# Optimization experiments

Measured on AMD Instinct MI355X. Metric: run time of the kernel, lower is better.

The kernel has to match this reference:

```python
import jax, jax.numpy as jnp
import numpy as np

B, S, D, H = 2, 2048, 1024, 16
DK = D // H

def setup_inputs() -> dict:
    key = jax.random.key(0)
    ks = jax.random.split(key, 11)
    s = 1.0 / np.sqrt(D)
    inp = {
        'q': jax.random.normal(ks[0], (B, S, D), jnp.float32),
        'k': jax.random.normal(ks[1], (B, S, D), jnp.float32),
        'v': jax.random.normal(ks[2], (B, S, D), jnp.float32),
        'mask': jnp.tril(jnp.ones((S, S), jnp.bool_))[None, None],  # [1,1,S,S] causal
        'w_q': jax.random.normal(ks[3], (D, D), jnp.float32) * s,
        'b_q': jax.random.normal(ks[4], (D,), jnp.float32) * s,
        'w_k': jax.random.normal(ks[5], (D, D), jnp.float32) * s,
        'b_k': jax.random.normal(ks[6], (D,), jnp.float32) * s,
        'w_v': jax.random.normal(ks[7], (D, D), jnp.float32) * s,
        'b_v': jax.random.normal(ks[8], (D,), jnp.float32) * s,
        'w_o': jax.random.normal(ks[9], (D, D), jnp.float32) * s,
        'b_o': jax.random.normal(ks[10], (D,), jnp.float32) * s,
    }
    return inp

def reference(q, k, v, mask, w_q, b_q, w_k, b_k, w_v, b_v, w_o, b_o):
    # Linear projections (torch Linear: x @ W^T + b)
    qh = (q @ w_q.T + b_q).reshape(B, S, H, DK).transpose(0, 2, 1, 3)  # [B,H,S,DK]
    kh = (k @ w_k.T + b_k).reshape(B, S, H, DK).transpose(0, 2, 1, 3)
    vh = (v @ w_v.T + b_v).reshape(B, S, H, DK).transpose(0, 2, 1, 3)
    scores = jnp.einsum('bhqd,bhkd->bhqk', qh, kh) / jnp.sqrt(jnp.float32(DK))
    scores = jnp.where(mask, scores, jnp.float32(-jnp.inf))
    attn = jax.nn.softmax(scores, axis=-1)  # dropout p=0.0 -> identity
    out = jnp.einsum('bhqk,bhkd->bhqd', attn, vh)
    out = out.transpose(0, 2, 1, 3).reshape(B, S, D)
    return out @ w_o.T + b_o
```

## Files before the change

kernel.cpp:

```cpp
#include <hip/hip_runtime.h>
#include <hip/hip_bf16.h>

typedef __bf16 bf16_t;
typedef __bf16 bf16x4 __attribute__((ext_vector_type(4)));
typedef __bf16 bf16x8 __attribute__((ext_vector_type(8)));
typedef float f32x4 __attribute__((ext_vector_type(4)));

#define B_ 2
#define S_ 2048
#define D_ 1024
#define H_ 16
#define DK_ 64
#define M_ (B_ * S_)

__device__ __forceinline__ f32x4 mfma16(bf16x8 a, bf16x8 b, f32x4 c) {
  return __builtin_amdgcn_mfma_f32_16x16x32_bf16(a, b, c, 0, 0, 0);
}

__device__ __forceinline__ void async_load16(const bf16_t* g, bf16_t* l) {
  __builtin_amdgcn_global_load_lds(
      (const __attribute__((address_space(1))) void*)g,
      (__attribute__((address_space(3))) void*)l, 16, 0, 0);
}


__global__ void cvt_all(const float* __restrict__ q, const float* __restrict__ k,
                        const float* __restrict__ v, const float* __restrict__ w0,
                        const float* __restrict__ w1, const float* __restrict__ w2,
                        const float* __restrict__ w3, bf16_t* __restrict__ qb,
                        bf16_t* __restrict__ kb, bf16_t* __restrict__ vb,
                        bf16_t* __restrict__ o0, bf16_t* __restrict__ o1,
                        bf16_t* __restrict__ o2, bf16_t* __restrict__ o3) {
  const int y = blockIdx.y;
  if (y >= 3 && blockIdx.x >= 512) return;
  const float* src;
  bf16_t* dst;
  float sc = 1.0f;
  switch (y) {
    case 0: src = q; dst = qb; break;
    case 1: src = k; dst = kb; break;
    case 2: src = v; dst = vb; break;
    case 3: src = w0; dst = o0; sc = 0.125f; break;
    case 4: src = w1; dst = o1; break;
    case 5: src = w2; dst = o2; break;
    default: src = w3; dst = o3; break;
  }
  long i = ((long)blockIdx.x * blockDim.x + threadIdx.x) * 8;
  const float4* s4 = (const float4*)(src + i);
  float4 a = s4[0], b = s4[1];
  bf16x8 o;
  o[0] = (bf16_t)(a.x * sc); o[1] = (bf16_t)(a.y * sc);
  o[2] = (bf16_t)(a.z * sc); o[3] = (bf16_t)(a.w * sc);
  o[4] = (bf16_t)(b.x * sc); o[5] = (bf16_t)(b.y * sc);
  o[6] = (bf16_t)(b.z * sc); o[7] = (bf16_t)(b.w * sc);
  *(bf16x8*)(dst + i) = o;
}


__device__ __forceinline__ int swzG(int b) {
  return b ^ (((b >> 7) & 7) << 4);
}

template <int NR>
__device__ __forceinline__ void stage_tile(const bf16_t* g, bf16_t* lds,
                                           const int* srcoff, int wave) {
#pragma unroll
  for (int rnd = 0; rnd < NR; ++rnd)
    async_load16(g + srcoff[rnd], lds + rnd * 2048 + wave * 512);
}

template <int MODE>
__device__ __forceinline__ void gemm_core(const bf16_t* __restrict__ A,
                                          const bf16_t* __restrict__ W,
                                          const float* __restrict__ bias,
                                          float bscale, void* __restrict__ Cv,
                                          bf16_t* __restrict__ As,
                                          bf16_t* __restrict__ Bs) {
  constexpr int N = 1024, K = 1024;
  constexpr int TILE = 128 * 64;
  const int tid = threadIdx.x;
  const int wave = tid >> 6, lane = tid & 63;
  const int quad = lane >> 4, l15 = lane & 15;
  const int wm = wave >> 1, wn = wave & 1;
  const int bm = blockIdx.x * 128, bn = blockIdx.y * 128;

  f32x4 acc[4][4] = {};

  int srcoff[4];
#pragma unroll
  for (int rnd = 0; rnd < 4; ++rnd) {
    const int bb = rnd * 4096 + tid * 16;
    const int sb = swzG(bb);
    srcoff[rnd] = (sb >> 7) * K + ((sb & 127) >> 1);
  }
  const bf16_t* ag = A + (long)bm * K;
  const bf16_t* bg = W + (long)bn * K;

  const int co0 = ((quad * 16) ^ ((l15 & 7) << 4)) >> 1;
  const int co1 = ((quad * 16 + 64) ^ ((l15 & 7) << 4)) >> 1;
  const int arow0 = (wm * 64 + l15) * 64;
  const int brow0 = (wn * 64 + l15) * 64;

  stage_tile<4>(ag, As, srcoff, wave);
  stage_tile<4>(bg, Bs, srcoff, wave);

  int cur = 0;
  for (int kk = 0; kk < K; kk += 64) {
    if (kk + 64 < K) {
      stage_tile<4>(ag + kk + 64, As + (cur ^ 1) * TILE, srcoff, wave);
      stage_tile<4>(bg + kk + 64, Bs + (cur ^ 1) * TILE, srcoff, wave);
      asm volatile("s_waitcnt vmcnt(8)" ::: "memory");
    } else {
      asm volatile("s_waitcnt vmcnt(0)" ::: "memory");
    }
    __builtin_amdgcn_sched_barrier(0);
    __builtin_amdgcn_s_barrier();
    __builtin_amdgcn_sched_barrier(0);

    const bf16_t* Ac = As + cur * TILE;
    const bf16_t* Bc = Bs + cur * TILE;
#pragma unroll
    for (int h = 0; h < 2; ++h) {
      const int co = h ? co1 : co0;
      bf16x8 af[4], bfr[4];
#pragma unroll
      for (int i = 0; i < 4; ++i)
        af[i] = *(const bf16x8*)&Ac[arow0 + i * 1024 + co];
#pragma unroll
      for (int i = 0; i < 4; ++i)
        bfr[i] = *(const bf16x8*)&Bc[brow0 + i * 1024 + co];
      __builtin_amdgcn_s_setprio(1);
#pragma unroll
      for (int mi = 0; mi < 4; ++mi)
#pragma unroll
        for (int ni = 0; ni < 4; ++ni)
          acc[mi][ni] = mfma16(af[mi], bfr[ni], acc[mi][ni]);
      __builtin_amdgcn_s_setprio(0);
    }

    asm volatile("s_waitcnt lgkmcnt(0)" ::: "memory");
    __builtin_amdgcn_sched_barrier(0);
    __builtin_amdgcn_s_barrier();
    __builtin_amdgcn_sched_barrier(0);
    cur ^= 1;
  }

#pragma unroll
  for (int mi = 0; mi < 4; ++mi) {
#pragma unroll
    for (int ni = 0; ni < 4; ++ni) {
      const int col = bn + wn * 64 + ni * 16 + l15;
      const float bsv = bias[col] * bscale;
      f32x4 v = acc[mi][ni];
      const int row0 = bm + wm * 64 + mi * 16 + quad * 4;
      if (MODE == 3) {
        float* C = (float*)Cv;
#pragma unroll
        for (int r = 0; r < 4; ++r)
          C[(long)(row0 + r) * N + col] = v[r] + bsv;
      } else if (MODE == 1) {
        bf16_t* C = (bf16_t*)Cv;
        const int hh = col >> 6, dk = col & 63;
        const int bq = row0 >> 11, s0 = row0 & 2047;
        bf16_t* base = C + (((long)bq * H_ + hh) * S_ + s0) * DK_ + dk;
#pragma unroll
        for (int r = 0; r < 4; ++r)
          base[(long)r * DK_] = (bf16_t)(v[r] + bsv);
      } else {
        bf16_t* C = (bf16_t*)Cv;
        const int hh = col >> 6, dk = col & 63;
        const int bq = row0 >> 11, s0 = row0 & 2047;
        bf16x4 pk;
#pragma unroll
        for (int r = 0; r < 4; ++r) pk[r] = (bf16_t)(v[r] + bsv);
        *(bf16x4*)(C + (((long)bq * H_ + hh) * DK_ + dk) * S_ + s0) = pk;
      }
    }
  }
}

__global__ __launch_bounds__(256) void gemm_qkv(
    const bf16_t* __restrict__ qb, const bf16_t* __restrict__ kb,
    const bf16_t* __restrict__ vb, const bf16_t* __restrict__ wq,
    const bf16_t* __restrict__ wk, const bf16_t* __restrict__ wv,
    const float* __restrict__ biq, const float* __restrict__ bik,
    const float* __restrict__ biv, bf16_t* __restrict__ Qh,
    bf16_t* __restrict__ Kh, bf16_t* __restrict__ Vt) {
  __shared__ bf16_t As[2][128 * 64];
  __shared__ bf16_t Bs[2][128 * 64];
  if (blockIdx.z == 0)
    gemm_core<1>(qb, wq, biq, 0.125f, Qh, &As[0][0], &Bs[0][0]);
  else if (blockIdx.z == 1)
    gemm_core<1>(kb, wk, bik, 1.0f, Kh, &As[0][0], &Bs[0][0]);
  else
    gemm_core<2>(vb, wv, biv, 1.0f, Vt, &As[0][0], &Bs[0][0]);
}

__global__ __launch_bounds__(256) void gemm_out64(
    const bf16_t* __restrict__ AO, const bf16_t* __restrict__ wo,
    const float* __restrict__ bo, float* __restrict__ out) {
  constexpr int N = 1024, K = 1024;
  __shared__ bf16_t As[2][64 * 64];
  __shared__ bf16_t Bs[2][128 * 64];
  const int tid = threadIdx.x;
  const int wave = tid >> 6, lane = tid & 63;
  const int quad = lane >> 4, l15 = lane & 15;
  const int wm = wave >> 1, wn = wave & 1;
  const int bm = blockIdx.x * 64, bn = blockIdx.y * 128;

  f32x4 acc[2][4] = {};

  int srcoff[4];
#pragma unroll
  for (int rnd = 0; rnd < 4; ++rnd) {
    const int bb = rnd * 4096 + tid * 16;
    const int sb = swzG(bb);
    srcoff[rnd] = (sb >> 7) * K + ((sb & 127) >> 1);
  }
  const bf16_t* ag = AO + (long)bm * K;
  const bf16_t* bg = wo + (long)bn * K;

  const int co0 = ((quad * 16) ^ ((l15 & 7) << 4)) >> 1;
  const int co1 = ((quad * 16 + 64) ^ ((l15 & 7) << 4)) >> 1;
  const int arow0 = (wm * 32 + l15) * 64;
  const int brow0 = (wn * 64 + l15) * 64;

  stage_tile<2>(ag, &As[0][0], srcoff, wave);
  stage_tile<4>(bg, &Bs[0][0], srcoff, wave);

  int cur = 0;
  for (int kk = 0; kk < K; kk += 64) {
    if (kk + 64 < K) {
      stage_tile<2>(ag + kk + 64, &As[cur ^ 1][0], srcoff, wave);
      stage_tile<4>(bg + kk + 64, &Bs[cur ^ 1][0], srcoff, wave);
      asm volatile("s_waitcnt vmcnt(6)" ::: "memory");
    } else {
      asm volatile("s_waitcnt vmcnt(0)" ::: "memory");
    }
    __builtin_amdgcn_sched_barrier(0);
    __builtin_amdgcn_s_barrier();
    __builtin_amdgcn_sched_barrier(0);

#pragma unroll
    for (int h = 0; h < 2; ++h) {
      const int co = h ? co1 : co0;
      bf16x8 af[2], bfr[4];
#pragma unroll
      for (int i = 0; i < 2; ++i)
        af[i] = *(const bf16x8*)&As[cur][arow0 + i * 1024 + co];
#pragma unroll
      for (int i = 0; i < 4; ++i)
        bfr[i] = *(const bf16x8*)&Bs[cur][brow0 + i * 1024 + co];
      __builtin_amdgcn_s_setprio(1);
#pragma unroll
      for (int mi = 0; mi < 2; ++mi)
#pragma unroll
        for (int ni = 0; ni < 4; ++ni)
          acc[mi][ni] = mfma16(af[mi], bfr[ni], acc[mi][ni]);
      __builtin_amdgcn_s_setprio(0);
    }

    asm volatile("s_waitcnt lgkmcnt(0)" ::: "memory");
    __builtin_amdgcn_sched_barrier(0);
    __builtin_amdgcn_s_barrier();
    __builtin_amdgcn_sched_barrier(0);
    cur ^= 1;
  }

#pragma unroll
  for (int mi = 0; mi < 2; ++mi) {
#pragma unroll
    for (int ni = 0; ni < 4; ++ni) {
      const int col = bn + wn * 64 + ni * 16 + l15;
      const float bsv = bo[col];
      f32x4 v = acc[mi][ni];
      const int row0 = bm + wm * 32 + mi * 16 + quad * 4;
#pragma unroll
      for (int r = 0; r < 4; ++r)
        out[(long)(row0 + r) * N + col] = v[r] + bsv;
    }
  }
}


__device__ __forceinline__ int swzK(int b) {
  return b ^ (((b >> 7) & 3) << 4) ^ (((b >> 10) & 1) << 6);
}
__device__ __forceinline__ int swzV(int b) {
  return b ^ (((b >> 7) & 7) << 4);
}

template <bool MASKED>
__device__ __forceinline__ void softmax_pa(const f32x4 st[4], float& l_i,
                                           bf16x8& pa0, bf16x8& pa1,
                                           const int qcol, const int quad) {
#pragma unroll
  for (int nb = 0; nb < 4; ++nb) {
    const int kvb = quad * 8 + (nb & 1) * 4 + (nb >> 1) * 32;
#pragma unroll
    for (int r = 0; r < 4; ++r) {
      float x = st[nb][r];
      if (MASKED && (kvb + r) > qcol) x = -30000.f;
      const float pv = __expf(x);
      l_i += pv;
      const bf16_t pb = (bf16_t)pv;
      const int idx = ((nb & 1) << 2) | r;
      if (nb < 2) pa0[idx] = pb;
      else        pa1[idx] = pb;
    }
  }
}

__global__ __launch_bounds__(256, 3) void flash_attn3(
    const bf16_t* __restrict__ Qh, const bf16_t* __restrict__ Kh,
    const bf16_t* __restrict__ Vt, bf16_t* __restrict__ Po,
    float* __restrict__ Pl) {
  const int bid = blockIdx.x;
  const int g = bid & 31;
  const int z = bid >> 5;
  const int i = z / 3, pi = z % 3;
  const int h = g & 15, b = g >> 4;
  const int tA = i, tB = 31 - i;
  const int tid = threadIdx.x, wave = tid >> 6, lane = tid & 63;
  const int quad = lane >> 4, l15 = lane & 15;
  const int qcol = wave * 16 + l15;
  const int prow = ((l15 >> 2) << 3) | (l15 & 3);

  __shared__ bf16_t Kls[2][64 * 64];
  __shared__ bf16_t Vls[2][64 * 64];

  const bf16_t* qhead = Qh + ((long)(b * H_ + h) * S_) * DK_;
  const bf16_t* khead = Kh + ((long)(b * H_ + h) * S_) * DK_;
  const bf16_t* vhead = Vt + ((long)(b * H_ + h) * DK_) * S_;

  int koffe[2], voffe[2], ldse[2];
#pragma unroll
  for (int c = 0; c < 2; ++c) {
    const int bb = c * 4096 + wave * 1024 + lane * 16;
    koffe[c] = swzK(bb) >> 1;
    const int vs = swzV(bb);
    voffe[c] = (vs >> 7) * S_ + ((vs & 127) >> 1);
    ldse[c] = c * 2048 + wave * 512;
  }

  int kro[4][2], vro[4][2];
#pragma unroll
  for (int nb = 0; nb < 4; ++nb) {
    const int krow = prow + (nb & 1) * 4 + (nb >> 1) * 32;
    const int vrow = nb * 16 + l15;
#pragma unroll
    for (int hh = 0; hh < 2; ++hh) {
      kro[nb][hh] = swzK(krow * 128 + quad * 16 + hh * 64) >> 1;
      vro[nb][hh] = swzV(vrow * 128 + quad * 16 + hh * 64) >> 1;
    }
  }

  const int qA = tA * 64 + wave * 16;
  const int qB = tB * 64 + wave * 16;
  const bf16_t* qpA = qhead + (long)(qA + l15) * DK_ + quad * 8;
  const bf16_t* qpB = qhead + (long)(qB + l15) * DK_ + quad * 8;
  const bf16x8 aqA0 = *(const bf16x8*)qpA;
  const bf16x8 aqA1 = *(const bf16x8*)(qpA + 32);
  const bf16x8 aqB0 = *(const bf16x8*)qpB;
  const bf16x8 aqB1 = *(const bf16x8*)(qpB + 32);

  f32x4 oA[4] = {}, oB[4] = {};
  float lA = 0.f, lB = 0.f;

  {
    const bf16_t* kt = khead + pi * (64 * DK_);
    const bf16_t* vt = vhead + pi * 64;
#pragma unroll
    for (int c = 0; c < 2; ++c) {
      async_load16(kt + koffe[c], &Kls[0][ldse[c]]);
      async_load16(vt + voffe[c], &Vls[0][ldse[c]]);
    }
  }

  int cur = 0;
  for (int j = pi; j <= tB; j += 3) {
    const bool pf = (j + 3 <= tB);
    if (pf) {
      const bf16_t* kt = khead + (j + 3) * (64 * DK_);
      const bf16_t* vt = vhead + (j + 3) * 64;
#pragma unroll
      for (int c = 0; c < 2; ++c) {
        async_load16(kt + koffe[c], &Kls[cur ^ 1][ldse[c]]);
        async_load16(vt + voffe[c], &Vls[cur ^ 1][ldse[c]]);
      }
      asm volatile("s_waitcnt vmcnt(4)" ::: "memory");
    } else {
      asm volatile("s_waitcnt vmcnt(0)" ::: "memory");
    }
    __builtin_amdgcn_sched_barrier(0);
    __builtin_amdgcn_s_barrier();
    __builtin_amdgcn_sched_barrier(0);

    const bf16_t* Kc = &Kls[cur][0];
    const bf16_t* Vc = &Vls[cur][0];

    bf16x8 k0[4], k1[4];
#pragma unroll
    for (int nb = 0; nb < 4; ++nb) {
      k0[nb] = *(const bf16x8*)&Kc[kro[nb][0]];
      k1[nb] = *(const bf16x8*)&Kc[kro[nb][1]];
    }

    bf16x8 paB0, paB1, paA0, paA1;
    {
      f32x4 stB[4];
#pragma unroll
      for (int nb = 0; nb < 4; ++nb) {
        f32x4 t = {};
        t = mfma16(k0[nb], aqB0, t);
        t = mfma16(k1[nb], aqB1, t);
        stB[nb] = t;
      }
      if (j == tB)
        softmax_pa<true>(stB, lB, paB0, paB1, qcol, quad);
      else
        softmax_pa<false>(stB, lB, paB0, paB1, qcol, quad);
    }
    const bool doA = (j <= tA);
    if (doA) {
      f32x4 stA[4];
#pragma unroll
      for (int nb = 0; nb < 4; ++nb) {
        f32x4 t = {};
        t = mfma16(k0[nb], aqA0, t);
        t = mfma16(k1[nb], aqA1, t);
        stA[nb] = t;
      }
      if (j == tA)
        softmax_pa<true>(stA, lA, paA0, paA1, qcol, quad);
      else
        softmax_pa<false>(stA, lA, paA0, paA1, qcol, quad);
    }

    bf16x8 v0[4], v1[4];
#pragma unroll
    for (int nb = 0; nb < 4; ++nb) {
      v0[nb] = *(const bf16x8*)&Vc[vro[nb][0]];
      v1[nb] = *(const bf16x8*)&Vc[vro[nb][1]];
    }
#pragma unroll
    for (int nb = 0; nb < 4; ++nb) {
      oB[nb] = mfma16(paB0, v0[nb], oB[nb]);
      oB[nb] = mfma16(paB1, v1[nb], oB[nb]);
    }
    if (doA) {
#pragma unroll
      for (int nb = 0; nb < 4; ++nb) {
        oA[nb] = mfma16(paA0, v0[nb], oA[nb]);
        oA[nb] = mfma16(paA1, v1[nb], oA[nb]);
      }
    }

    asm volatile("s_waitcnt lgkmcnt(0)" ::: "memory");
    __builtin_amdgcn_sched_barrier(0);
    __builtin_amdgcn_s_barrier();
    __builtin_amdgcn_sched_barrier(0);
    cur ^= 1;
  }

  lA += __shfl_xor(lA, 16, 64);
  lA += __shfl_xor(lA, 32, 64);
  lB += __shfl_xor(lB, 16, 64);
  lB += __shfl_xor(lB, 32, 64);

  bf16_t* po = Po + (long)pi * (M_ * D_);
  bf16_t* poA = po + (long)(b * S_ + qA + quad * 4) * D_ + h * DK_ + l15;
  bf16_t* poB = po + (long)(b * S_ + qB + quad * 4) * D_ + h * DK_ + l15;
#pragma unroll
  for (int r = 0; r < 4; ++r) {
#pragma unroll
    for (int nb = 0; nb < 4; ++nb) {
      poA[(long)r * D_ + nb * 16] = (bf16_t)oA[nb][r];
      poB[(long)r * D_ + nb * 16] = (bf16_t)oB[nb][r];
    }
  }

  if (quad == 0) {
    float* pl = Pl + (long)pi * (B_ * H_ * S_) + (long)(b * H_ + h) * S_;
    pl[qA + l15] = lA;
    pl[qB + l15] = lB;
  }
}


__global__ __launch_bounds__(256) void merge_po(const bf16_t* __restrict__ Po,
                                                const float* __restrict__ Pl,
                                                bf16_t* __restrict__ AO) {
  const long e = ((long)blockIdx.x * 256 + threadIdx.x) * 8;
  const int bs = (int)(e >> 10);
  const int d = (int)(e & 1023);
  const int h = d >> 6;
  const int b = bs >> 11, s = bs & 2047;
  const long lidx = ((long)(b * H_ + h)) * S_ + s;

  float acc[8] = {0.f, 0.f, 0.f, 0.f, 0.f, 0.f, 0.f, 0.f};
  float L = 0.f;
#pragma unroll
  for (int p = 0; p < 3; ++p) {
    bf16x8 x = *(const bf16x8*)(Po + (long)p * (M_ * D_) + e);
#pragma unroll
    for (int k = 0; k < 8; ++k) acc[k] += (float)x[k];
    L += Pl[(long)p * (B_ * H_ * S_) + lidx];
  }
  const float inv = 1.f / L;
  bf16x8 y;
#pragma unroll
  for (int k = 0; k < 8; ++k) y[k] = (bf16_t)(acc[k] * inv);
  *(bf16x8*)(AO + e) = y;
}


extern "C" void kernel_launch(void* const* d_in, const int* in_sizes, int n_in,
                              void* d_out, int out_size, void* d_ws, size_t ws_size,
                              hipStream_t stream) {
  const float* q = (const float*)d_in[0];
  const float* k = (const float*)d_in[1];
  const float* v = (const float*)d_in[2];
  const float* wq = (const float*)d_in[4];
  const float* bq = (const float*)d_in[5];
  const float* wk = (const float*)d_in[6];
  const float* bk = (const float*)d_in[7];
  const float* wv = (const float*)d_in[8];
  const float* bv = (const float*)d_in[9];
  const float* wo = (const float*)d_in[10];
  const float* bo = (const float*)d_in[11];
  float* out = (float*)d_out;

  char* ws = (char*)d_ws;
  const size_t MB = 1024 * 1024;
  bf16_t* Qh = (bf16_t*)(ws);
  bf16_t* Kh = (bf16_t*)(ws + 8 * MB);
  bf16_t* Vt = (bf16_t*)(ws + 16 * MB);
  bf16_t* AO = (bf16_t*)(ws + 24 * MB);
  bf16_t* qb = (bf16_t*)(ws + 32 * MB);
  bf16_t* kb = (bf16_t*)(ws + 40 * MB);
  bf16_t* vb = (bf16_t*)(ws + 48 * MB);
  bf16_t* wqb = (bf16_t*)(ws + 56 * MB);
  bf16_t* wkb = (bf16_t*)(ws + 58 * MB);
  bf16_t* wvb = (bf16_t*)(ws + 60 * MB);
  bf16_t* wob = (bf16_t*)(ws + 62 * MB);
  bf16_t* Po = (bf16_t*)(ws + 32 * MB);
  float* Pl = (float*)(ws + 56 * MB);

  cvt_all<<<dim3(2048, 7, 1), 256, 0, stream>>>(q, k, v, wq, wk, wv, wo, qb, kb,
                                                vb, wqb, wkb, wvb, wob);
  gemm_qkv<<<dim3(32, 8, 3), 256, 0, stream>>>(qb, kb, vb, wqb, wkb, wvb, bq, bk,
                                               bv, Qh, Kh, Vt);
  flash_attn3<<<dim3(1536, 1, 1), 256, 0, stream>>>(Qh, Kh, Vt, Po, Pl);
  merge_po<<<dim3(2048, 1, 1), 256, 0, stream>>>(Po, Pl, AO);
  gemm_out64<<<dim3(64, 8, 1), 256, 0, stream>>>(AO, wob, bo, out);
}
```

Measured before the change: 217.9 us.

## Halve QKV GEMM K-tile to 32 with new LDS swizzle layout

The QKV projection GEMM now stages 128x32 tiles per K step instead of 128x64, halving its LDS footprint. It uses a new 64-byte-row swizzle and single-pass fragment loads. The output GEMM keeps the old 128-byte swizzle, now through a renamed helper. The aim is likely higher occupancy from less shared memory, at the cost of twice as many barrier-synchronised iterations with less MFMA work in each.

```diff
diff --git a/kernel.cpp b/kernel.cpp
--- a/kernel.cpp
+++ b/kernel.cpp
@@ -77,7 +77,7 @@
                                           bf16_t* __restrict__ As,
                                           bf16_t* __restrict__ Bs) {
   constexpr int N = 1024, K = 1024;
-  constexpr int TILE = 128 * 64;
+  constexpr int TILE = 128 * 32;
   const int tid = threadIdx.x;
   const int wave = tid >> 6, lane = tid & 63;
   const int quad = lane >> 4, l15 = lane & 15;
@@ -86,30 +86,29 @@
 
   f32x4 acc[4][4] = {};
 
-  int srcoff[4];
-#pragma unroll
-  for (int rnd = 0; rnd < 4; ++rnd) {
+  int srcoff[2];
+#pragma unroll
+  for (int rnd = 0; rnd < 2; ++rnd) {
     const int bb = rnd * 4096 + tid * 16;
     const int sb = swzG(bb);
-    srcoff[rnd] = (sb >> 7) * K + ((sb & 127) >> 1);
+    srcoff[rnd] = (sb >> 6) * K + ((sb & 63) >> 1);
   }
   const bf16_t* ag = A + (long)bm * K;
   const bf16_t* bg = W + (long)bn * K;
 
-  const int co0 = ((quad * 16) ^ ((l15 & 7) << 4)) >> 1;
-  const int co1 = ((quad * 16 + 64) ^ ((l15 & 7) << 4)) >> 1;
-  const int arow0 = (wm * 64 + l15) * 64;
-  const int brow0 = (wn * 64 + l15) * 64;
-
-  stage_tile<4>(ag, As, srcoff, wave);
-  stage_tile<4>(bg, Bs, srcoff, wave);
+  const int xorv = ((l15 >> 1) & 7) << 4;
+  const int aco = (((wm * 64 + l15) * 64 + quad * 16) ^ xorv) >> 1;
+  const int bco = (((wn * 64 + l15) * 64 + quad * 16) ^ xorv) >> 1;
+
+  stage_tile<2>(ag, As, srcoff, wave);
+  stage_tile<2>(bg, Bs, srcoff, wave);
 
   int cur = 0;
-  for (int kk = 0; kk < K; kk += 64) {
-    if (kk + 64 < K) {
-      stage_tile<4>(ag + kk + 64, As + (cur ^ 1) * TILE, srcoff, wave);
-      stage_tile<4>(bg + kk + 64, Bs + (cur ^ 1) * TILE, srcoff, wave);
-      asm volatile("s_waitcnt vmcnt(8)" ::: "memory");
+  for (int kk = 0; kk < K; kk += 32) {
+    if (kk + 32 < K) {
+      stage_tile<2>(ag + kk + 32, As + (cur ^ 1) * TILE, srcoff, wave);
+      stage_tile<2>(bg + kk + 32, Bs + (cur ^ 1) * TILE, srcoff, wave);
+      asm volatile("s_waitcnt vmcnt(4)" ::: "memory");
     } else {
       asm volatile("s_waitcnt vmcnt(0)" ::: "memory");
     }
@@ -119,24 +118,20 @@
 
     const bf16_t* Ac = As + cur * TILE;
     const bf16_t* Bc = Bs + cur * TILE;
-#pragma unroll
-    for (int h = 0; h < 2; ++h) {
-      const int co = h ? co1 : co0;
-      bf16x8 af[4], bfr[4];
-#pragma unroll
-      for (int i = 0; i < 4; ++i)
-        af[i] = *(const bf16x8*)&Ac[arow0 + i * 1024 + co];
-#pragma unroll
-      for (int i = 0; i < 4; ++i)
-        bfr[i] = *(const bf16x8*)&Bc[brow0 + i * 1024 + co];
-      __builtin_amdgcn_s_setprio(1);
-#pragma unroll
-      for (int mi = 0; mi < 4; ++mi)
-#pragma unroll
-        for (int ni = 0; ni < 4; ++ni)
-          acc[mi][ni] = mfma16(af[mi], bfr[ni], acc[mi][ni]);
-      __builtin_amdgcn_s_setprio(0);
-    }
+    bf16x8 af[4], bfr[4];
+#pragma unroll
+    for (int i = 0; i < 4; ++i)
+      af[i] = *(const bf16x8*)&Ac[aco + i * 512];
+#pragma unroll
+    for (int i = 0; i < 4; ++i)
+      bfr[i] = *(const bf16x8*)&Bc[bco + i * 512];
+    __builtin_amdgcn_s_setprio(1);
+#pragma unroll
+    for (int mi = 0; mi < 4; ++mi)
+#pragma unroll
+      for (int ni = 0; ni < 4; ++ni)
+        acc[mi][ni] = mfma16(af[mi], bfr[ni], acc[mi][ni]);
+    __builtin_amdgcn_s_setprio(0);
 
     asm volatile("s_waitcnt lgkmcnt(0)" ::: "memory");
     __builtin_amdgcn_sched_barrier(0);
@@ -186,14 +181,26 @@
     const float* __restrict__ biq, const float* __restrict__ bik,
     const float* __restrict__ biv, bf16_t* __restrict__ Qh,
     bf16_t* __restrict__ Kh, bf16_t* __restrict__ Vt) {
-  __shared__ bf16_t As[2][128 * 64];
-  __shared__ bf16_t Bs[2][128 * 64];
+  __shared__ bf16_t As[2][128 * 32];
+  __shared__ bf16_t Bs[2][128 * 32];
   if (blockIdx.z == 0)
     gemm_core<1>(qb, wq, biq, 0.125f, Qh, &As[0][0], &Bs[0][0]);
   else if (blockIdx.z == 1)
     gemm_core<1>(kb, wk, bik, 1.0f, Kh, &As[0][0], &Bs[0][0]);
   else
     gemm_core<2>(vb, wv, biv, 1.0f, Vt, &As[0][0], &Bs[0][0]);
+}
+
+__device__ __forceinline__ int swzG128(int b) {
+  return b ^ (((b >> 7) & 7) << 4);
+}
+
+template <int NR>
+__device__ __forceinline__ void stage_tile128(const bf16_t* g, bf16_t* lds,
+                                              const int* srcoff, int wave) {
+#pragma unroll
+  for (int rnd = 0; rnd < NR; ++rnd)
+    async_load16(g + srcoff[rnd], lds + rnd * 2048 + wave * 512);
 }
 
 __global__ __launch_bounds__(256) void gemm_out64(
@@ -214,7 +221,7 @@
 #pragma unroll
   for (int rnd = 0; rnd < 4; ++rnd) {
     const int bb = rnd * 4096 + tid * 16;
-    const int sb = swzG(bb);
+    const int sb = swzG128(bb);
     srcoff[rnd] = (sb >> 7) * K + ((sb & 127) >> 1);
   }
   const bf16_t* ag = AO + (long)bm * K;
@@ -225,14 +232,14 @@
   const int arow0 = (wm * 32 + l15) * 64;
   const int brow0 = (wn * 64 + l15) * 64;
 
-  stage_tile<2>(ag, &As[0][0], srcoff, wave);
-  stage_tile<4>(bg, &Bs[0][0], srcoff, wave);
+  stage_tile128<2>(ag, &As[0][0], srcoff, wave);
+  stage_tile128<4>(bg, &Bs[0][0], srcoff, wave);
 
   int cur = 0;
   for (int kk = 0; kk < K; kk += 64) {
     if (kk + 64 < K) {
-      stage_tile<2>(ag + kk + 64, &As[cur ^ 1][0], srcoff, wave);
-      stage_tile<4>(bg + kk + 64, &Bs[cur ^ 1][0], srcoff, wave);
+      stage_tile128<2>(ag + kk + 64, &As[cur ^ 1][0], srcoff, wave);
+      stage_tile128<4>(bg + kk + 64, &Bs[cur ^ 1][0], srcoff, wave);
       asm volatile("s_waitcnt vmcnt(6)" ::: "memory");
     } else {
       asm volatile("s_waitcnt vmcnt(0)" ::: "memory");
```

After: 214.5 us. No clear change (-1.6%).
